# Kernel tuning notes

Measured on AMD Instinct MI355X. Metric: run time of the kernel, lower is better.

The kernel has to match this reference:

```python
import jax, jax.numpy as jnp
import numpy as np

H = 512
IN = 512
B = 64
T = 256
EPS = 1e-8


def _clin(x, Wr, Wi, br, bi):
    # complex linear: (Wr + i Wi)(xr + i xi) + (br + i bi); x: (B, F, 2)
    xr, xi = x[..., 0], x[..., 1]
    yr = xr @ Wr.T - xi @ Wi.T + br
    yi = xr @ Wi.T + xi @ Wr.T + bi
    return jnp.stack([yr, yi], axis=-1)


def _mod_apply(fn, z):
    # modulus nonlinearity: fn(|z|) * z / |z|
    m = jnp.sqrt(z[..., 0] ** 2 + z[..., 1] ** 2)
    s = fn(m) / (m + EPS)
    return z * s[..., None]


def _cmul(a, b):
    ar, ai = a[..., 0], a[..., 1]
    br, bi = b[..., 0], b[..., 1]
    return jnp.stack([ar * br - ai * bi, ai * br + ar * bi], axis=-1)


def _layer(x_tbf2, p):
    Wri, Wii, bri, bii, Wrh, Wih, brh, bih = p
    b = x_tbf2.shape[1]
    h0 = jnp.zeros((b, H, 2), x_tbf2.dtype)
    c0 = jnp.zeros((b, H, 2), x_tbf2.dtype)

    def step(carry, x_t):
        h, c = carry
        pre = _clin(x_t, Wri, Wii, bri, bii) + _clin(h, Wrh, Wih, brh, bih)
        gates = _mod_apply(jax.nn.sigmoid, pre[:, :3 * H])
        g_t = _mod_apply(jnp.tanh, pre[:, 3 * H:])
        i_t = gates[:, :H]
        f_t = gates[:, H:2 * H]
        o_t = gates[:, 2 * H:]
        # NOTE: cell update uses componentwise (real) multiply, matching torch.mul
        c_t = c * f_t + i_t * g_t
        # hidden update uses true complex multiply, matching self.mul
        h_t = _cmul(o_t, _mod_apply(jnp.tanh, c_t))
        return (h_t, c_t), h_t

    (hT, cT), ys = jax.lax.scan(step, (h0, c0), x_tbf2)
    return ys, hT, cT


def setup_inputs() -> dict:
    key = jax.random.key(0)
    ks = jax.random.split(key, 20)
    std = 1.0 / np.sqrt(H)

    def u(k, shape):
        return jax.random.uniform(k, shape, jnp.float32, -std, std)

    inp = {"x": jax.random.normal(ks[0], (B, T, IN, 2), jnp.float32)}
    idx = 1
    for l, fin in enumerate([IN, H]):
        for name, shape in [("i2h_Wr", (4 * H, fin)), ("i2h_Wi", (4 * H, fin)),
                            ("i2h_br", (4 * H,)), ("i2h_bi", (4 * H,)),
                            ("h2h_Wr", (4 * H, H)), ("h2h_Wi", (4 * H, H)),
                            ("h2h_br", (4 * H,)), ("h2h_bi", (4 * H,))]:
            inp[f"{name}_{l}"] = u(ks[idx], shape)
            idx += 1
    return inp


def reference(x,
              i2h_Wr_0, i2h_Wi_0, i2h_br_0, i2h_bi_0,
              h2h_Wr_0, h2h_Wi_0, h2h_br_0, h2h_bi_0,
              i2h_Wr_1, i2h_Wi_1, i2h_br_1, i2h_bi_1,
              h2h_Wr_1, h2h_Wi_1, h2h_br_1, h2h_bi_1):
    # x: (B, T, IN, 2), batch_first -> (T, B, IN, 2)
    xt = jnp.transpose(x, (1, 0, 2, 3))
    p0 = (i2h_Wr_0, i2h_Wi_0, i2h_br_0, i2h_bi_0, h2h_Wr_0, h2h_Wi_0, h2h_br_0, h2h_bi_0)
    p1 = (i2h_Wr_1, i2h_Wi_1, i2h_br_1, i2h_bi_1, h2h_Wr_1, h2h_Wi_1, h2h_br_1, h2h_bi_1)
    ys, h0, c0 = _layer(xt, p0)
    ys, h1, c1 = _layer(ys, p1)
    y = jnp.transpose(ys, (1, 0, 2, 3))  # (B, T, H, 2)
    h = jnp.stack([h0, h1], axis=0)      # (num_layers, B, H, 2)
    c = jnp.stack([c0, c1], axis=0)
    return (y, (h, c))
```

## Files before the change

kernel.cpp:

```cpp
#include <hip/hip_runtime.h>
#include <hip/hip_bf16.h>

typedef _Float16 f16;
typedef _Float16 f16x8 __attribute__((ext_vector_type(8)));
typedef float f32x4 __attribute__((ext_vector_type(4)));

#define T_ 256
#define SC 2048.0f
#define INV_SC (1.0f / 2048.0f)
#define RMASK 15
#define NSTAGE 258
#define MFMA(A, B, C)  __builtin_amdgcn_mfma_f32_16x16x32_f16(A, B, C, 0, 0, 0)


__global__ void prepack_x_kernel(const float* __restrict__ x, f16* __restrict__ X0) {
  unsigned int idx = blockIdx.x * 256 + threadIdx.x;
  int e    = idx & 7;
  int l    = (idx >> 3) & 63;
  int part = (idx >> 9) & 1;
  int ks   = (idx >> 10) & 31;
  int mt   = (idx >> 15) & 3;
  int t    = idx >> 17;
  int m = mt * 16 + (l & 15);
  int k = ks * 32 + ((l >> 4) << 3) + e;
  int cc = k >> 9, kw = k & 511;
  float v = x[(((size_t)m * T_ + t) * 512 + kw) * 2 + cc];
  f16 h = (f16)v;
  X0[idx] = part ? (f16)((v - (float)h) * SC) : h;
}

__global__ void prepack_w_kernel(const float* __restrict__ Wri, const float* __restrict__ Wii,
                                 const float* __restrict__ Wrh, const float* __restrict__ Wih,
                                 f16* __restrict__ out) {
  unsigned int idx = blockIdx.x * 256 + threadIdx.x;
  int e     = idx & 7;
  int l     = (idx >> 3) & 63;
  int ks    = (idx >> 9) & 63;
  int nt    = (idx >> 15) & 1;
  int jb    = (idx >> 16) & 127;
  int which = idx >> 23;
  int n_local = nt * 16 + (l & 15);
  int np = jb * 32 + n_local;
  int j  = np >> 3;
  int g  = (np >> 1) & 3;
  int cc = np & 1;
  int k  = ks * 32 + ((l >> 4) << 3) + e;
  int kb = k >> 9, kw = k & 511;
  size_t s = (size_t)(g * 512 + j) * 512 + kw;
  float v;
  if (cc == 0) v = (kb == 0) ? Wri[s] : (kb == 1) ? -Wii[s] : (kb == 2) ? Wrh[s] : -Wih[s];
  else         v = (kb == 0) ? Wii[s] : (kb == 1) ?  Wri[s] : (kb == 2) ? Wih[s] :  Wrh[s];
  f16 h = (f16)v;
  out[idx] = which ? (f16)((v - (float)h) * SC) : h;
}

struct PersistArgs {
  const f16* X0;
  f16* ys0;
  f16* h1;
  const f16* Wpk0;
  const f16* Wpk1;
  const float *br10, *bi10, *br20, *bi20;
  const float *br11, *bi11, *br21, *bi21;
  float* y;
  float* hout;
  float* cout;
  unsigned* flags;
};

__global__ __launch_bounds__(1024, 4) void lstm_persist(PersistArgs a) {
  extern __shared__ char smem[];
  f16* Wl = (f16*)smem;
  float* redf = (float*)(smem + 131072);
  volatile unsigned* goLds = (volatile unsigned*)(smem + 148480);

  int bid = blockIdx.x;
  int xcd = bid & 7, rr = bid >> 3;
  int lay = rr & 1;
  int jb = (rr >> 1) * 8 + xcd;
  int tid = threadIdx.x;
  int w = tid >> 6, l = tid & 63;
  int mt = w & 3, kq = w >> 2;
  int n_loc = l & 15, r0 = (l >> 4) * 4;
  bool carrier = (kq >= 2);

  int em = tid >> 2, ejl = tid & 3;
  int emt = em >> 4, eml = em & 15;
  int jg = jb * 4 + ejl;

  const f16* Wpk = lay ? a.Wpk1 : a.Wpk0;
  const f16* WhiG = Wpk + (size_t)jb * 65536;
  const f16* WloG = Wpk + 8388608 + (size_t)jb * 65536;
  for (int i = tid * 8; i < 65536; i += 8192)
    *reinterpret_cast<f16x8*>(Wl + i) = *reinterpret_cast<const f16x8*>(WhiG + i);
  if (tid == 0) *goLds = 0u;

  float bsr[4], bsi[4];
  {
    const float* br1 = lay ? a.br11 : a.br10;
    const float* bi1 = lay ? a.bi11 : a.bi10;
    const float* br2 = lay ? a.br21 : a.br20;
    const float* bi2 = lay ? a.bi21 : a.bi20;
#pragma unroll
    for (int g = 0; g < 4; ++g) {
      int nb = g * 512 + jg;
      bsr[g] = br1[nb] + br2[nb];
      bsi[g] = bi1[nb] + bi2[nb];
    }
  }
  __syncthreads();

  const f32x4 z4 = {0.f, 0.f, 0.f, 0.f};
  f32x4 xm0 = z4, xs0 = z4, xm1 = z4, xs1 = z4;

  if (carrier && lay == 0) {
    int ksl = (kq - 2) * 16;
    const f16* pa = a.X0 + mt * 32768 + ksl * 1024 + l * 8;
    const f16* pw = Wl + ksl * 512 + l * 8;
    const f16* po = WloG + ksl * 512 + l * 8;
#pragma unroll 4
    for (int i = 0; i < 16; ++i) {
      f16x8 ah = *reinterpret_cast<const f16x8*>(pa + i * 1024);
      f16x8 al = *reinterpret_cast<const f16x8*>(pa + i * 1024 + 512);
      f16x8 w0 = *reinterpret_cast<const f16x8*>(pw + i * 512);
      f16x8 w1 = *reinterpret_cast<const f16x8*>(pw + 32768 + i * 512);
      f16x8 o0 = *reinterpret_cast<const f16x8*>(po + i * 512);
      f16x8 o1 = *reinterpret_cast<const f16x8*>(po + 32768 + i * 512);
      xm0 = MFMA(ah, w0, xm0); xs0 = MFMA(al, w0, xs0); xs0 = MFMA(ah, o0, xs0);
      xm1 = MFMA(ah, w1, xm1); xs1 = MFMA(al, w1, xs1); xs1 = MFMA(ah, o1, xs1);
    }
  }

  float c_r = 0.f, c_i = 0.f;

  for (int s = 0; s < NSTAGE; ++s) {
    bool active = lay ? (s >= 2) : (s < T_);
    int t = lay ? (s - 2) : s;

    if (s > 0) {
      if (w == 0) {
        const unsigned* fp = a.flags + l * 4;
        for (;;) {
          unsigned f0 = __hip_atomic_load(fp + 0, __ATOMIC_RELAXED, __HIP_MEMORY_SCOPE_AGENT);
          unsigned f1 = __hip_atomic_load(fp + 1, __ATOMIC_RELAXED, __HIP_MEMORY_SCOPE_AGENT);
          unsigned f2 = __hip_atomic_load(fp + 2, __ATOMIC_RELAXED, __HIP_MEMORY_SCOPE_AGENT);
          unsigned f3 = __hip_atomic_load(fp + 3, __ATOMIC_RELAXED, __HIP_MEMORY_SCOPE_AGENT);
          unsigned mn = min(min(f0, f1), min(f2, f3));
          if (__all(mn >= (unsigned)s)) break;
          __builtin_amdgcn_s_sleep(1);
        }
        if (l == 0) { asm volatile("" ::: "memory"); *goLds = (unsigned)s; }
      } else {
        while (*goLds < (unsigned)s) __builtin_amdgcn_s_sleep(1);
      }
      asm volatile("" ::: "memory");
    }

    f32x4 comb0 = z4, comb1 = z4;
    int rb0 = 0, rb1 = 0;
    if (active) {
      f32x4 acc0  = carrier ? xm0 : z4;
      f32x4 sacc0 = carrier ? xs0 : z4;
      f32x4 acc1  = carrier ? xm1 : z4;
      f32x4 sacc1 = carrier ? xs1 : z4;
      if (t > 0) {
        const f16* Ab = (lay ? a.h1 : a.ys0) + (size_t)((t - 1) & RMASK) * 131072;
        int ksl = kq * 8;
        int ksg = 32 + kq * 8;
        const f16* pa = Ab + mt * 32768 + ksl * 1024 + l * 8;
        const f16* pw = Wl + ksg * 512 + l * 8;
        const f16* po = WloG + ksg * 512 + l * 8;
#pragma unroll
        for (int i = 0; i < 8; ++i) {
          f16x8 ah = *reinterpret_cast<const f16x8*>(pa + i * 1024);
          f16x8 al = *reinterpret_cast<const f16x8*>(pa + i * 1024 + 512);
          f16x8 w0 = *reinterpret_cast<const f16x8*>(pw + i * 512);
          f16x8 w1 = *reinterpret_cast<const f16x8*>(pw + 32768 + i * 512);
          f16x8 o0 = *reinterpret_cast<const f16x8*>(po + i * 512);
          f16x8 o1 = *reinterpret_cast<const f16x8*>(po + 32768 + i * 512);
          acc0 = MFMA(ah, w0, acc0); sacc0 = MFMA(al, w0, sacc0); sacc0 = MFMA(ah, o0, sacc0);
          acc1 = MFMA(ah, w1, acc1); sacc1 = MFMA(al, w1, sacc1); sacc1 = MFMA(ah, o1, sacc1);
        }
      }
      comb0 = acc0 + sacc0 * INV_SC;
      comb1 = acc1 + sacc1 * INV_SC;
      rb0 = (((kq >> 1) * 4 + mt) * 2 + 0) * 272 + n_loc * 17 + r0;
      rb1 = (((kq >> 1) * 4 + mt) * 2 + 1) * 272 + n_loc * 17 + r0;
      if ((kq & 1) == 0) {
#pragma unroll
        for (int q = 0; q < 4; ++q) { redf[rb0 + q] = comb0[q]; redf[rb1 + q] = comb1[q]; }
      }
    }
    __syncthreads();
    if (active && (kq & 1)) {
#pragma unroll
      for (int q = 0; q < 4; ++q) { redf[rb0 + q] += comb0[q]; redf[rb1 + q] += comb1[q]; }
    }
    __syncthreads();

    float hr = 0.f, him = 0.f, cnr = 0.f, cni = 0.f;
    if (active && tid < 256) {
      float zr[4], zi[4];
#pragma unroll
      for (int g = 0; g < 4; ++g) {
        int nl = ejl * 8 + g * 2;
        int nt_ = nl >> 4, nn = nl & 15;
        int i0 = (emt * 2 + nt_) * 272 + nn * 17 + eml;
        int i1 = ((4 + emt) * 2 + nt_) * 272 + nn * 17 + eml;
        zr[g] = redf[i0] + redf[i1] + bsr[g];
        zi[g] = redf[i0 + 17] + redf[i1 + 17] + bsi[g];
      }
      float gr[4], gi[4];
#pragma unroll
      for (int g = 0; g < 4; ++g) {
        float mag = sqrtf(zr[g] * zr[g] + zi[g] * zi[g]);
        float fn = (g < 3) ? (1.f / (1.f + __expf(-mag))) : tanhf(mag);
        float sg = fn / (mag + 1e-8f);
        gr[g] = zr[g] * sg;
        gi[g] = zi[g] * sg;
      }
      cnr = c_r * gr[1] + gr[0] * gr[3];
      cni = c_i * gi[1] + gi[0] * gi[3];
      c_r = cnr; c_i = cni;
      float mm = sqrtf(cnr * cnr + cni * cni);
      float sg = tanhf(mm) / (mm + 1e-8f);
      float dr = cnr * sg, di = cni * sg;
      hr  = gr[2] * dr - gi[2] * di;
      him = gi[2] * dr + gr[2] * di;

      f16 h0 = (f16)hr, h2 = (f16)him;
      unsigned a1 = (unsigned)__builtin_bit_cast(unsigned short, h0)
                  | ((unsigned)__builtin_bit_cast(unsigned short, (f16)((hr - (float)h0) * SC)) << 16);
      unsigned a2 = (unsigned)__builtin_bit_cast(unsigned short, h2)
                  | ((unsigned)__builtin_bit_cast(unsigned short, (f16)((him - (float)h2) * SC)) << 16);
      unsigned b1 = __shfl_xor(a1, 1, 64);
      unsigned b2 = __shfl_xor(a2, 1, 64);
      unsigned v0, v1; int kbase;
      int p = ejl >> 1;
      if ((ejl & 1) == 0) {
        v0 = (a1 & 0xffffu) | (b1 << 16);
        v1 = (a1 >> 16) | (b1 & 0xffff0000u);
        kbase = jb * 4 + 2 * p;
      } else {
        v0 = (b2 & 0xffffu) | (a2 << 16);
        v1 = (b2 >> 16) | (a2 & 0xffff0000u);
        kbase = 512 + jb * 4 + 2 * p;
      }
      f16* Yb = (lay ? a.h1 : a.ys0) + (size_t)(t & RMASK) * 131072;
      unsigned* Y32 = (unsigned*)Yb;
      int ks2 = kbase >> 5;
      int lane_h = eml + 16 * ((kbase >> 3) & 3);
      int e0 = kbase & 7;
      int idx0 = ((emt * 32 + ks2) * 2 + 0) * 512 + lane_h * 8 + e0;
      int idx1 = ((emt * 32 + ks2) * 2 + 1) * 512 + lane_h * 8 + e0;
      __hip_atomic_store(&Y32[idx0 >> 1], v0, __ATOMIC_RELAXED, __HIP_MEMORY_SCOPE_AGENT);
      __hip_atomic_store(&Y32[idx1 >> 1], v1, __ATOMIC_RELAXED, __HIP_MEMORY_SCOPE_AGENT);
    }

    asm volatile("s_waitcnt vmcnt(0)" ::: "memory");
    __syncthreads();
    if (tid == 0 && s + 1 < NSTAGE)
      __hip_atomic_store(&a.flags[bid], (unsigned)(s + 1),
                         __ATOMIC_RELAXED, __HIP_MEMORY_SCOPE_AGENT);

    if (carrier) {
      xm0 = z4; xs0 = z4; xm1 = z4; xs1 = z4;
      bool nextAct = lay ? (s + 1 >= 2 && s + 1 < NSTAGE) : (s + 1 < T_);
      if (nextAct) {
        int tn = lay ? (s - 1) : (s + 1);
        const f16* Ab = lay ? (a.ys0 + (size_t)(tn & RMASK) * 131072)
                            : (a.X0 + (size_t)tn * 131072);
        int ksl = (kq - 2) * 16;
        const f16* pa = Ab + mt * 32768 + ksl * 1024 + l * 8;
        const f16* pw = Wl + ksl * 512 + l * 8;
        const f16* po = WloG + ksl * 512 + l * 8;
#pragma unroll 4
        for (int i = 0; i < 16; ++i) {
          f16x8 ah = *reinterpret_cast<const f16x8*>(pa + i * 1024);
          f16x8 al = *reinterpret_cast<const f16x8*>(pa + i * 1024 + 512);
          f16x8 w0 = *reinterpret_cast<const f16x8*>(pw + i * 512);
          f16x8 w1 = *reinterpret_cast<const f16x8*>(pw + 32768 + i * 512);
          f16x8 o0 = *reinterpret_cast<const f16x8*>(po + i * 512);
          f16x8 o1 = *reinterpret_cast<const f16x8*>(po + 32768 + i * 512);
          xm0 = MFMA(ah, w0, xm0); xs0 = MFMA(al, w0, xs0); xs0 = MFMA(ah, o0, xs0);
          xm1 = MFMA(ah, w1, xm1); xs1 = MFMA(al, w1, xs1); xs1 = MFMA(ah, o1, xs1);
        }
      }
    }

    if (active && tid < 256) {
      if (lay) {
        float2 yv; yv.x = hr; yv.y = him;
        *reinterpret_cast<float2*>(a.y + (((size_t)em * T_ + t) * 512 + jg) * 2) = yv;
      }
      if (t == T_ - 1) {
        float* hp = a.hout + (size_t)lay * 65536 + ((size_t)em * 512 + jg) * 2;
        hp[0] = hr; hp[1] = him;
        float* cq = a.cout + (size_t)lay * 65536 + ((size_t)em * 512 + jg) * 2;
        cq[0] = cnr; cq[1] = cni;
      }
    }
  }
}

extern "C" void kernel_launch(void* const* d_in, const int* in_sizes, int n_in,
                              void* d_out, int out_size, void* d_ws, size_t ws_size,
                              hipStream_t stream) {
  const float* x = (const float*)d_in[0];
  char* ws = (char*)d_ws;
  f16* X0   = (f16*)(ws + 0);
  f16* Wpk0 = (f16*)(ws + (size_t)67108864);
  f16* Wpk1 = (f16*)(ws + (size_t)100663296);
  f16* ys0  = (f16*)(ws + (size_t)134217728);
  f16* h1   = (f16*)(ws + (size_t)138412032);
  unsigned* flags = (unsigned*)(ws + (size_t)142606336);

  hipMemsetAsync(ws + 142606336, 0, 1024, stream);

  prepack_x_kernel<<<131072, 256, 0, stream>>>(x, X0);
  prepack_w_kernel<<<65536, 256, 0, stream>>>((const float*)d_in[1], (const float*)d_in[2],
                                              (const float*)d_in[5], (const float*)d_in[6], Wpk0);
  prepack_w_kernel<<<65536, 256, 0, stream>>>((const float*)d_in[9], (const float*)d_in[10],
                                              (const float*)d_in[13], (const float*)d_in[14], Wpk1);

  float* y = (float*)d_out;
  PersistArgs pa;
  pa.X0 = X0; pa.ys0 = ys0; pa.h1 = h1;
  pa.Wpk0 = Wpk0; pa.Wpk1 = Wpk1;
  pa.br10 = (const float*)d_in[3];  pa.bi10 = (const float*)d_in[4];
  pa.br20 = (const float*)d_in[7];  pa.bi20 = (const float*)d_in[8];
  pa.br11 = (const float*)d_in[11]; pa.bi11 = (const float*)d_in[12];
  pa.br21 = (const float*)d_in[15]; pa.bi21 = (const float*)d_in[16];
  pa.y = y; pa.hout = y + 16777216; pa.cout = y + 16777216 + 131072;
  pa.flags = flags;

  hipFuncSetAttribute((const void*)lstm_persist,
                      hipFuncAttributeMaxDynamicSharedMemorySize, 148608);
  void* kargs[] = { &pa };
  hipLaunchCooperativeKernel((const void*)lstm_persist, dim3(256), dim3(1024),
                             kargs, 148608, stream);
}
```

Measured before the change: 3.985 ms.

## Overlap epilogue with next-step input GEMM across waves and drop block barrier

The gate/cell epilogue is restricted to the four kq==0 waves, and the other twelve waves now share the next timestep's input-projection GEMM (11/11/10 k-slices), where eight waves did it before. The block-wide barrier before publishing the step flag is replaced by an LDS atomic counter, so the last epilogue wave to finish signals completion. This lets epilogue work and the input GEMM run concurrently and takes one __syncthreads off the serial recurrence. The cost is an uneven k split and reliance on the LDS counter for correct ordering.

```diff
diff --git a/kernel.cpp b/kernel.cpp
--- a/kernel.cpp
+++ b/kernel.cpp
@@ -68,11 +68,34 @@
   unsigned* flags;
 };
 
+__device__ __forceinline__ void xgemm_part(const f16* __restrict__ Ab,
+                                           const f16* __restrict__ WhiL,
+                                           const f16* __restrict__ WloG,
+                                           int mt, int ks0, int cnt, int l,
+                                           f32x4& xm0, f32x4& xs0,
+                                           f32x4& xm1, f32x4& xs1) {
+  const f16* pa = Ab + mt * 32768 + ks0 * 1024 + l * 8;
+  const f16* pw = WhiL + ks0 * 512 + l * 8;
+  const f16* po = WloG + ks0 * 512 + l * 8;
+#pragma unroll 4
+  for (int i = 0; i < cnt; ++i) {
+    f16x8 ah = *reinterpret_cast<const f16x8*>(pa + i * 1024);
+    f16x8 al = *reinterpret_cast<const f16x8*>(pa + i * 1024 + 512);
+    f16x8 w0 = *reinterpret_cast<const f16x8*>(pw + i * 512);
+    f16x8 w1 = *reinterpret_cast<const f16x8*>(pw + 32768 + i * 512);
+    f16x8 o0 = *reinterpret_cast<const f16x8*>(po + i * 512);
+    f16x8 o1 = *reinterpret_cast<const f16x8*>(po + 32768 + i * 512);
+    xm0 = MFMA(ah, w0, xm0); xs0 = MFMA(al, w0, xs0); xs0 = MFMA(ah, o0, xs0);
+    xm1 = MFMA(ah, w1, xm1); xs1 = MFMA(al, w1, xs1); xs1 = MFMA(ah, o1, xs1);
+  }
+}
+
 __global__ __launch_bounds__(1024, 4) void lstm_persist(PersistArgs a) {
   extern __shared__ char smem[];
   f16* Wl = (f16*)smem;
   float* redf = (float*)(smem + 131072);
   volatile unsigned* goLds = (volatile unsigned*)(smem + 148480);
+  unsigned* ectr = (unsigned*)(smem + 148484);
 
   int bid = blockIdx.x;
   int xcd = bid & 7, rr = bid >> 3;
@@ -82,7 +105,9 @@
   int w = tid >> 6, l = tid & 63;
   int mt = w & 3, kq = w >> 2;
   int n_loc = l & 15, r0 = (l >> 4) * 4;
-  bool carrier = (kq >= 2);
+  bool carrier = (kq >= 1);
+  int xks0 = (kq == 1) ? 0 : (kq == 2) ? 11 : 22;
+  int xcnt = (kq == 3) ? 10 : 11;
 
   int em = tid >> 2, ejl = tid & 3;
   int emt = em >> 4, eml = em & 15;
@@ -93,7 +118,7 @@
   const f16* WloG = Wpk + 8388608 + (size_t)jb * 65536;
   for (int i = tid * 8; i < 65536; i += 8192)
     *reinterpret_cast<f16x8*>(Wl + i) = *reinterpret_cast<const f16x8*>(WhiG + i);
-  if (tid == 0) *goLds = 0u;
+  if (tid == 0) { *goLds = 0u; *ectr = 0u; }
 
   float bsr[4], bsi[4];
   {
@@ -113,23 +138,8 @@
   const f32x4 z4 = {0.f, 0.f, 0.f, 0.f};
   f32x4 xm0 = z4, xs0 = z4, xm1 = z4, xs1 = z4;
 
-  if (carrier && lay == 0) {
-    int ksl = (kq - 2) * 16;
-    const f16* pa = a.X0 + mt * 32768 + ksl * 1024 + l * 8;
-    const f16* pw = Wl + ksl * 512 + l * 8;
-    const f16* po = WloG + ksl * 512 + l * 8;
-#pragma unroll 4
-    for (int i = 0; i < 16; ++i) {
-      f16x8 ah = *reinterpret_cast<const f16x8*>(pa + i * 1024);
-      f16x8 al = *reinterpret_cast<const f16x8*>(pa + i * 1024 + 512);
-      f16x8 w0 = *reinterpret_cast<const f16x8*>(pw + i * 512);
-      f16x8 w1 = *reinterpret_cast<const f16x8*>(pw + 32768 + i * 512);
-      f16x8 o0 = *reinterpret_cast<const f16x8*>(po + i * 512);
-      f16x8 o1 = *reinterpret_cast<const f16x8*>(po + 32768 + i * 512);
-      xm0 = MFMA(ah, w0, xm0); xs0 = MFMA(al, w0, xs0); xs0 = MFMA(ah, o0, xs0);
-      xm1 = MFMA(ah, w1, xm1); xs1 = MFMA(al, w1, xs1); xs1 = MFMA(ah, o1, xs1);
-    }
-  }
+  if (carrier && lay == 0)
+    xgemm_part(a.X0, Wl, WloG, mt, xks0, xcnt, l, xm0, xs0, xm1, xs1);
 
   float c_r = 0.f, c_i = 0.f;
 
@@ -198,106 +208,93 @@
     }
     __syncthreads();
 
-    float hr = 0.f, him = 0.f, cnr = 0.f, cni = 0.f;
-    if (active && tid < 256) {
-      float zr[4], zi[4];
-#pragma unroll
-      for (int g = 0; g < 4; ++g) {
-        int nl = ejl * 8 + g * 2;
-        int nt_ = nl >> 4, nn = nl & 15;
-        int i0 = (emt * 2 + nt_) * 272 + nn * 17 + eml;
-        int i1 = ((4 + emt) * 2 + nt_) * 272 + nn * 17 + eml;
-        zr[g] = redf[i0] + redf[i1] + bsr[g];
-        zi[g] = redf[i0 + 17] + redf[i1 + 17] + bsi[g];
-      }
-      float gr[4], gi[4];
-#pragma unroll
-      for (int g = 0; g < 4; ++g) {
-        float mag = sqrtf(zr[g] * zr[g] + zi[g] * zi[g]);
-        float fn = (g < 3) ? (1.f / (1.f + __expf(-mag))) : tanhf(mag);
-        float sg = fn / (mag + 1e-8f);
-        gr[g] = zr[g] * sg;
-        gi[g] = zi[g] * sg;
-      }
-      cnr = c_r * gr[1] + gr[0] * gr[3];
-      cni = c_i * gi[1] + gi[0] * gi[3];
-      c_r = cnr; c_i = cni;
-      float mm = sqrtf(cnr * cnr + cni * cni);
-      float sg = tanhf(mm) / (mm + 1e-8f);
-      float dr = cnr * sg, di = cni * sg;
-      hr  = gr[2] * dr - gi[2] * di;
-      him = gi[2] * dr + gr[2] * di;
-
-      f16 h0 = (f16)hr, h2 = (f16)him;
-      unsigned a1 = (unsigned)__builtin_bit_cast(unsigned short, h0)
-                  | ((unsigned)__builtin_bit_cast(unsigned short, (f16)((hr - (float)h0) * SC)) << 16);
-      unsigned a2 = (unsigned)__builtin_bit_cast(unsigned short, h2)
-                  | ((unsigned)__builtin_bit_cast(unsigned short, (f16)((him - (float)h2) * SC)) << 16);
-      unsigned b1 = __shfl_xor(a1, 1, 64);
-      unsigned b2 = __shfl_xor(a2, 1, 64);
-      unsigned v0, v1; int kbase;
-      int p = ejl >> 1;
-      if ((ejl & 1) == 0) {
-        v0 = (a1 & 0xffffu) | (b1 << 16);
-        v1 = (a1 >> 16) | (b1 & 0xffff0000u);
-        kbase = jb * 4 + 2 * p;
-      } else {
-        v0 = (b2 & 0xffffu) | (a2 << 16);
-        v1 = (b2 >> 16) | (a2 & 0xffff0000u);
-        kbase = 512 + jb * 4 + 2 * p;
-      }
-      f16* Yb = (lay ? a.h1 : a.ys0) + (size_t)(t & RMASK) * 131072;
-      unsigned* Y32 = (unsigned*)Yb;
-      int ks2 = kbase >> 5;
-      int lane_h = eml + 16 * ((kbase >> 3) & 3);
-      int e0 = kbase & 7;
-      int idx0 = ((emt * 32 + ks2) * 2 + 0) * 512 + lane_h * 8 + e0;
-      int idx1 = ((emt * 32 + ks2) * 2 + 1) * 512 + lane_h * 8 + e0;
-      __hip_atomic_store(&Y32[idx0 >> 1], v0, __ATOMIC_RELAXED, __HIP_MEMORY_SCOPE_AGENT);
-      __hip_atomic_store(&Y32[idx1 >> 1], v1, __ATOMIC_RELAXED, __HIP_MEMORY_SCOPE_AGENT);
-    }
-
-    asm volatile("s_waitcnt vmcnt(0)" ::: "memory");
-    __syncthreads();
-    if (tid == 0 && s + 1 < NSTAGE)
-      __hip_atomic_store(&a.flags[bid], (unsigned)(s + 1),
-                         __ATOMIC_RELAXED, __HIP_MEMORY_SCOPE_AGENT);
-
-    if (carrier) {
+    if (kq == 0) {
+      float hr = 0.f, him = 0.f, cnr = 0.f, cni = 0.f;
+      if (active) {
+        float zr[4], zi[4];
+#pragma unroll
+        for (int g = 0; g < 4; ++g) {
+          int nl = ejl * 8 + g * 2;
+          int nt_ = nl >> 4, nn = nl & 15;
+          int i0 = (emt * 2 + nt_) * 272 + nn * 17 + eml;
+          int i1 = ((4 + emt) * 2 + nt_) * 272 + nn * 17 + eml;
+          zr[g] = redf[i0] + redf[i1] + bsr[g];
+          zi[g] = redf[i0 + 17] + redf[i1 + 17] + bsi[g];
+        }
+        float gr[4], gi[4];
+#pragma unroll
+        for (int g = 0; g < 4; ++g) {
+          float mag = sqrtf(zr[g] * zr[g] + zi[g] * zi[g]);
+          float fn = (g < 3) ? (1.f / (1.f + __expf(-mag))) : tanhf(mag);
+          float sg = fn / (mag + 1e-8f);
+          gr[g] = zr[g] * sg;
+          gi[g] = zi[g] * sg;
+        }
+        cnr = c_r * gr[1] + gr[0] * gr[3];
+        cni = c_i * gi[1] + gi[0] * gi[3];
+        c_r = cnr; c_i = cni;
+        float mm = sqrtf(cnr * cnr + cni * cni);
+        float sg = tanhf(mm) / (mm + 1e-8f);
+        float dr = cnr * sg, di = cni * sg;
+        hr  = gr[2] * dr - gi[2] * di;
+        him = gi[2] * dr + gr[2] * di;
+
+        f16 h0 = (f16)hr, h2 = (f16)him;
+        unsigned a1 = (unsigned)__builtin_bit_cast(unsigned short, h0)
+                    | ((unsigned)__builtin_bit_cast(unsigned short, (f16)((hr - (float)h0) * SC)) << 16);
+        unsigned a2 = (unsigned)__builtin_bit_cast(unsigned short, h2)
+                    | ((unsigned)__builtin_bit_cast(unsigned short, (f16)((him - (float)h2) * SC)) << 16);
+        unsigned b1 = __shfl_xor(a1, 1, 64);
+        unsigned b2 = __shfl_xor(a2, 1, 64);
+        unsigned v0, v1; int kbase;
+        int p = ejl >> 1;
+        if ((ejl & 1) == 0) {
+          v0 = (a1 & 0xffffu) | (b1 << 16);
+          v1 = (a1 >> 16) | (b1 & 0xffff0000u);
+          kbase = jb * 4 + 2 * p;
+        } else {
+          v0 = (b2 & 0xffffu) | (a2 << 16);
+          v1 = (b2 >> 16) | (a2 & 0xffff0000u);
+          kbase = 512 + jb * 4 + 2 * p;
+        }
+        f16* Yb = (lay ? a.h1 : a.ys0) + (size_t)(t & RMASK) * 131072;
+        unsigned* Y32 = (unsigned*)Yb;
+        int ks2 = kbase >> 5;
+        int lane_h = eml + 16 * ((kbase >> 3) & 3);
+        int e0 = kbase & 7;
+        int idx0 = ((emt * 32 + ks2) * 2 + 0) * 512 + lane_h * 8 + e0;
+        int idx1 = ((emt * 32 + ks2) * 2 + 1) * 512 + lane_h * 8 + e0;
+        __hip_atomic_store(&Y32[idx0 >> 1], v0, __ATOMIC_RELAXED, __HIP_MEMORY_SCOPE_AGENT);
+        __hip_atomic_store(&Y32[idx1 >> 1], v1, __ATOMIC_RELAXED, __HIP_MEMORY_SCOPE_AGENT);
+      }
+      asm volatile("s_waitcnt vmcnt(0)" ::: "memory");
+      if (l == 0) {
+        unsigned old = __hip_atomic_fetch_add(ectr, 1u, __ATOMIC_ACQ_REL,
+                                              __HIP_MEMORY_SCOPE_WORKGROUP);
+        if ((old & 3u) == 3u && s + 1 < NSTAGE)
+          __hip_atomic_store(&a.flags[bid], (unsigned)(s + 1),
+                             __ATOMIC_RELAXED, __HIP_MEMORY_SCOPE_AGENT);
+      }
+      if (active) {
+        if (lay) {
+          float2 yv; yv.x = hr; yv.y = him;
+          *reinterpret_cast<float2*>(a.y + (((size_t)em * T_ + t) * 512 + jg) * 2) = yv;
+        }
+        if (t == T_ - 1) {
+          float* hp = a.hout + (size_t)lay * 65536 + ((size_t)em * 512 + jg) * 2;
+          hp[0] = hr; hp[1] = him;
+          float* cq = a.cout + (size_t)lay * 65536 + ((size_t)em * 512 + jg) * 2;
+          cq[0] = cnr; cq[1] = cni;
+        }
+      }
+    } else {
       xm0 = z4; xs0 = z4; xm1 = z4; xs1 = z4;
       bool nextAct = lay ? (s + 1 >= 2 && s + 1 < NSTAGE) : (s + 1 < T_);
       if (nextAct) {
         int tn = lay ? (s - 1) : (s + 1);
         const f16* Ab = lay ? (a.ys0 + (size_t)(tn & RMASK) * 131072)
                             : (a.X0 + (size_t)tn * 131072);
-        int ksl = (kq - 2) * 16;
-        const f16* pa = Ab + mt * 32768 + ksl * 1024 + l * 8;
-        const f16* pw = Wl + ksl * 512 + l * 8;
-        const f16* po = WloG + ksl * 512 + l * 8;
-#pragma unroll 4
-        for (int i = 0; i < 16; ++i) {
-          f16x8 ah = *reinterpret_cast<const f16x8*>(pa + i * 1024);
-          f16x8 al = *reinterpret_cast<const f16x8*>(pa + i * 1024 + 512);
-          f16x8 w0 = *reinterpret_cast<const f16x8*>(pw + i * 512);
-          f16x8 w1 = *reinterpret_cast<const f16x8*>(pw + 32768 + i * 512);
-          f16x8 o0 = *reinterpret_cast<const f16x8*>(po + i * 512);
-          f16x8 o1 = *reinterpret_cast<const f16x8*>(po + 32768 + i * 512);
-          xm0 = MFMA(ah, w0, xm0); xs0 = MFMA(al, w0, xs0); xs0 = MFMA(ah, o0, xs0);
-          xm1 = MFMA(ah, w1, xm1); xs1 = MFMA(al, w1, xs1); xs1 = MFMA(ah, o1, xs1);
-        }
-      }
-    }
-
-    if (active && tid < 256) {
-      if (lay) {
-        float2 yv; yv.x = hr; yv.y = him;
-        *reinterpret_cast<float2*>(a.y + (((size_t)em * T_ + t) * 512 + jg) * 2) = yv;
-      }
-      if (t == T_ - 1) {
-        float* hp = a.hout + (size_t)lay * 65536 + ((size_t)em * 512 + jg) * 2;
-        hp[0] = hr; hp[1] = him;
-        float* cq = a.cout + (size_t)lay * 65536 + ((size_t)em * 512 + jg) * 2;
-        cq[0] = cnr; cq[1] = cni;
+        xgemm_part(Ab, Wl, WloG, mt, xks0, xcnt, l, xm0, xs0, xm1, xs1);
       }
     }
   }
```

Result: slower. 4.163 ms (+4.5%).
